# Kernel optimization log

Measured on AMD Instinct MI355X. Metric: run time of the kernel, lower is better.

The kernel has to match this reference:

```python
import jax, jax.numpy as jnp
import numpy as np

N_NODES = 50000
N_EDGES = 600000
D = 128
EPS = 1e-5
AVG_D_LOG = float(np.log(4 + 1))  # avg_d={'log': log(avg_d+1)}, avg_d=4


def setup_inputs() -> dict:
    key = jax.random.key(0)
    ks = jax.random.split(key, 8)
    h = jax.random.normal(ks[0], (N_NODES, D), dtype=jnp.float32)
    # guarantee every node has at least one incoming edge (self-loop)
    edge_dst = jnp.concatenate([
        jnp.arange(N_NODES, dtype=jnp.int64),
        jax.random.randint(ks[1], (N_EDGES - N_NODES,), 0, N_NODES).astype(jnp.int64),
    ])
    edge_src = jax.random.randint(ks[2], (N_EDGES,), 0, N_NODES).astype(jnp.int64)
    def lin(k, fan_in, fan_out):
        lim = 1.0 / np.sqrt(fan_in)
        return jax.random.uniform(k, (fan_in, fan_out), jnp.float32, -lim, lim)
    W_pre = lin(ks[3], 2 * D, D)
    b_pre = jnp.zeros((D,), jnp.float32)
    W_post = lin(ks[4], 12 * D + D, D)  # 4 aggregators * 3 scalers * D + in_dim
    b_post = jnp.zeros((D,), jnp.float32)
    W_mix = lin(ks[5], D, D)
    b_mix = jnp.zeros((D,), jnp.float32)
    return {"h": h, "edge_src": edge_src, "edge_dst": edge_dst,
            "W_pre": W_pre, "b_pre": b_pre, "W_post": W_post,
            "b_post": b_post, "W_mix": W_mix, "b_mix": b_mix}


def reference(h, edge_src, edge_dst, W_pre, b_pre, W_post, b_post, W_mix, b_mix):
    n = h.shape[0]
    # pretrans_edges: cat(src, dst) -> Linear -> ReLU (MLP act) -> ReLU (outer)
    z2 = jnp.concatenate([h[edge_src], h[edge_dst]], axis=1)        # [E, 2D]
    e = jax.nn.relu(z2 @ W_pre + b_pre)                             # [E, D]
    # multi-aggregator segment reduce over destination nodes
    deg = jax.ops.segment_sum(jnp.ones_like(edge_dst, jnp.float32), edge_dst, n)  # [N]
    inv_deg = 1.0 / deg[:, None]
    mean = jax.ops.segment_sum(e, edge_dst, n) * inv_deg
    mean_sq = jax.ops.segment_sum(e * e, edge_dst, n) * inv_deg
    std = jnp.sqrt(jax.nn.relu(mean_sq - mean * mean) + EPS)
    mx = jax.ops.segment_max(e, edge_dst, n)
    mn = jax.ops.segment_min(e, edge_dst, n)
    agg = jnp.concatenate([mean, mx, mn, std], axis=1)              # [N, 4D]
    # scalers: identity, amplification, attenuation
    log_d = jnp.log(deg + 1.0)[:, None]
    scaled = jnp.concatenate([agg, agg * (log_d / AVG_D_LOG), agg * (AVG_D_LOG / log_d)], axis=1)  # [N, 12D]
    # posttrans: cat(h, aggregated) -> Linear -> ReLU
    hp = jax.nn.relu(jnp.concatenate([h, scaled], axis=1) @ W_post + b_post)  # [N, D]
    # mixing network + residual (node_dim == out_dim)
    out = h + jax.nn.leaky_relu(hp @ W_mix + b_mix, negative_slope=0.01)
    return out
```

## Files before the change

kernel.cpp:

```cpp
#include <hip/hip_runtime.h>
#include <hip/hip_bf16.h>

#define N_NODES 50000
#define N_EDGES 600000
#define D 128
#define NB_SCAN 196

constexpr float AVG_D_LOG = 1.6094379124341003f;
constexpr float EPS_V = 1e-5f;

#define PQ_B     0ul
#define AGG_B    25600000ul
#define HBF_B    76800000ul
#define WPRET2_B 89600000ul
#define WPOSTT_B 89665536ul
#define WMIXT_B  90091520ul
#define DEGC_B   90124288ul
#define OFF_B    90324288ul
#define CUR_B    90524352ul
#define SRCS_B   90724352ul
#define BSUM_B   93124352ul

typedef __attribute__((ext_vector_type(8))) short bf16x8;
typedef __attribute__((ext_vector_type(4))) float f32x4;

__device__ __forceinline__ short f2b(float f) {
    unsigned u = __builtin_bit_cast(unsigned, f);
    u += 0x7fffu + ((u >> 16) & 1u);
    return (short)(u >> 16);
}
__device__ __forceinline__ unsigned pk2(float a, float b) {
    return (unsigned)(unsigned short)f2b(a) | ((unsigned)(unsigned short)f2b(b) << 16);
}
__device__ __forceinline__ float blo(unsigned u) { return __uint_as_float(u << 16); }
__device__ __forceinline__ float bhi(unsigned u) { return __uint_as_float(u & 0xffff0000u); }

__global__ __launch_bounds__(256) void prep_kernel(
    const float* __restrict__ h, const float* __restrict__ Wpre,
    const float* __restrict__ Wpost, const float* __restrict__ Wmix,
    short* __restrict__ hbf, short* __restrict__ wpreT2,
    short* __restrict__ wpostT, short* __restrict__ wmixT,
    int* __restrict__ degc, int* __restrict__ cursor)
{
    long i = (long)blockIdx.x * 256 + threadIdx.x;
    if (i < 6400000) { hbf[i] = f2b(h[i]); return; }
    i -= 6400000;
    if (i < 32768) {
        int n = i >> 7, k = i & 127;
        float v = (n < 128) ? Wpre[k * 128 + n] : Wpre[(k + 128) * 128 + (n - 128)];
        wpreT2[n * 128 + k] = f2b(v);
        return;
    }
    i -= 32768;
    if (i < 212992) { int k = i >> 7, n = i & 127; wpostT[n * 1664 + k] = f2b(Wpost[k * 128 + n]); return; }
    i -= 212992;
    if (i < 16384) { int k = i >> 7, n = i & 127; wmixT[n * 128 + k] = f2b(Wmix[k * 128 + n]); return; }
    i -= 16384;
    if (i < N_NODES) { degc[i] = 0; return; }
    i -= N_NODES;
    if (i < N_NODES) cursor[i] = 0;
}

__global__ __launch_bounds__(256) void hist_kernel(const int* __restrict__ edst, int* __restrict__ degc) {
    int e = blockIdx.x * 256 + threadIdx.x;
    if (e < N_EDGES) atomicAdd(&degc[edst[e]], 1);
}

__global__ __launch_bounds__(256) void scan1_kernel(const int* __restrict__ degc, int* __restrict__ bsum) {
    int n = blockIdx.x * 256 + threadIdx.x;
    int v = (n < N_NODES) ? degc[n] : 0;
#pragma unroll
    for (int o = 32; o > 0; o >>= 1) v += __shfl_down(v, o);
    __shared__ int w4[4];
    if ((threadIdx.x & 63) == 0) w4[threadIdx.x >> 6] = v;
    __syncthreads();
    if (threadIdx.x == 0) bsum[blockIdx.x] = w4[0] + w4[1] + w4[2] + w4[3];
}

__global__ __launch_bounds__(256) void scan2_kernel(int* __restrict__ bsum, int* __restrict__ off) {
    __shared__ int sd[256];
    int tid = threadIdx.x;
    int v = (tid < NB_SCAN) ? bsum[tid] : 0;
    sd[tid] = v;
    __syncthreads();
    for (int o = 1; o < 256; o <<= 1) {
        int t = (tid >= o) ? sd[tid - o] : 0;
        __syncthreads();
        sd[tid] += t;
        __syncthreads();
    }
    if (tid < NB_SCAN) bsum[tid] = sd[tid] - v;
    if (tid == 0) off[N_NODES] = sd[255];
}

__global__ __launch_bounds__(256) void scan3_kernel(const int* __restrict__ degc,
                                                    const int* __restrict__ bsum, int* __restrict__ off) {
    __shared__ int sd[256];
    int tid = threadIdx.x;
    int n = blockIdx.x * 256 + tid;
    int v = (n < N_NODES) ? degc[n] : 0;
    sd[tid] = v;
    __syncthreads();
    for (int o = 1; o < 256; o <<= 1) {
        int t = (tid >= o) ? sd[tid - o] : 0;
        __syncthreads();
        sd[tid] += t;
        __syncthreads();
    }
    if (n < N_NODES) off[n] = sd[tid] - v + bsum[blockIdx.x];
}

__global__ __launch_bounds__(256) void scatter_kernel(const int* __restrict__ esrc, const int* __restrict__ edst,
                                                      const int* __restrict__ off, int* __restrict__ cursor,
                                                      int* __restrict__ srcs) {
    int e = blockIdx.x * 256 + threadIdx.x;
    if (e < N_EDGES) {
        int d = edst[e];
        int p = off[d] + atomicAdd(&cursor[d], 1);
        srcs[p] = esrc[e];
    }
}

__global__ __launch_bounds__(256) void gemm_pq_kernel(
    const short* __restrict__ hbf, const short* __restrict__ wpreT2,
    const float* __restrict__ bpre, short* __restrict__ PQ)
{
    __shared__ __align__(16) short As[128][72];
    __shared__ __align__(16) short Bs[256][72];

    const int tid = threadIdx.x;
    const int bn = blockIdx.x * 128;
    const int lane = tid & 63, wv = tid >> 6;
    const int lm = lane & 15, quad = lane >> 4;

    f32x4 acc[2][16];
#pragma unroll
    for (int a = 0; a < 2; a++)
#pragma unroll
        for (int b = 0; b < 16; b++) acc[a][b] = (f32x4){0.f, 0.f, 0.f, 0.f};

#pragma unroll
    for (int kc = 0; kc < 2; kc++) {
        __syncthreads();
#pragma unroll
        for (int t = 0; t < 4; t++) {
            int q = tid + t * 256;
            int m = q >> 3, seg = q & 7;
            int n = bn + m; if (n >= N_NODES) n = N_NODES - 1;
            *(int4*)&As[m][seg * 8] = *(const int4*)(hbf + (long)n * 128 + kc * 64 + seg * 8);
        }
#pragma unroll
        for (int t = 0; t < 8; t++) {
            int q = tid + t * 256;
            int n = q >> 3, seg = q & 7;
            *(int4*)&Bs[n][seg * 8] = *(const int4*)(wpreT2 + n * 128 + kc * 64 + seg * 8);
        }
        __syncthreads();
#pragma unroll
        for (int ks = 0; ks < 2; ks++) {
            const int ko = ks * 32 + quad * 8;
            bf16x8 a0 = *(const bf16x8*)&As[wv * 32 + lm][ko];
            bf16x8 a1 = *(const bf16x8*)&As[wv * 32 + 16 + lm][ko];
#pragma unroll
            for (int ct = 0; ct < 16; ct++) {
                bf16x8 b = *(const bf16x8*)&Bs[ct * 16 + lm][ko];
                acc[0][ct] = __builtin_amdgcn_mfma_f32_16x16x32_bf16(b, a0, acc[0][ct], 0, 0, 0);
                acc[1][ct] = __builtin_amdgcn_mfma_f32_16x16x32_bf16(b, a1, acc[1][ct], 0, 0, 0);
            }
        }
    }

#pragma unroll
    for (int rt = 0; rt < 2; rt++) {
        int row = wv * 32 + rt * 16 + lm;
        int n = bn + row;
        if (n >= N_NODES) continue;
        short* dst = PQ + (long)n * 256;
#pragma unroll
        for (int ct = 0; ct < 16; ct++) {
            int col = ct * 16 + quad * 4;
            float v0 = acc[rt][ct][0], v1 = acc[rt][ct][1], v2 = acc[rt][ct][2], v3 = acc[rt][ct][3];
            if (ct >= 8) {
                float4 bv = *(const float4*)(bpre + (col - 128));
                v0 += bv.x; v1 += bv.y; v2 += bv.z; v3 += bv.w;
            }
            int2 pkd; pkd.x = (int)pk2(v0, v1); pkd.y = (int)pk2(v2, v3);
            *(int2*)(dst + col) = pkd;
        }
    }
}

__global__ __launch_bounds__(256) void edgestats_kernel(
    const short* __restrict__ PQ, const int* __restrict__ srcs,
    const int* __restrict__ off, short* __restrict__ aggbf)
{
    const int wv = threadIdx.x >> 6, lane = threadIdx.x & 63;
    const int n = blockIdx.x * 4 + wv;
    const unsigned* Pb = (const unsigned*)PQ;

    const int s0 = __builtin_amdgcn_readfirstlane(off[n]);
    const int s1 = __builtin_amdgcn_readfirstlane(off[n + 1]);

    unsigned qu = Pb[(long)n * 128 + 64 + lane];
    const float qa = blo(qu), qb = bhi(qu);

    float sA = 0.f, sB = 0.f, qA = 0.f, qB = 0.f;
    float mxA = -1e30f, mxB = -1e30f, mnA = 1e30f, mnB = 1e30f;

    int p = s0;
    for (; p + 4 <= s1; p += 4) {
        int i0 = srcs[p], i1 = srcs[p + 1], i2 = srcs[p + 2], i3 = srcs[p + 3];
        unsigned u0 = Pb[(long)i0 * 128 + lane];
        unsigned u1 = Pb[(long)i1 * 128 + lane];
        unsigned u2 = Pb[(long)i2 * 128 + lane];
        unsigned u3 = Pb[(long)i3 * 128 + lane];
#pragma unroll
        for (int j = 0; j < 4; j++) {
            unsigned u = (j == 0) ? u0 : (j == 1) ? u1 : (j == 2) ? u2 : u3;
            float a = blo(u) + qa; a = a > 0.f ? a : 0.f;
            float b = bhi(u) + qb; b = b > 0.f ? b : 0.f;
            sA += a; sB += b; qA += a * a; qB += b * b;
            mxA = fmaxf(mxA, a); mxB = fmaxf(mxB, b);
            mnA = fminf(mnA, a); mnB = fminf(mnB, b);
        }
    }
    for (; p < s1; p++) {
        unsigned u = Pb[(long)srcs[p] * 128 + lane];
        float a = blo(u) + qa; a = a > 0.f ? a : 0.f;
        float b = bhi(u) + qb; b = b > 0.f ? b : 0.f;
        sA += a; sB += b; qA += a * a; qB += b * b;
        mxA = fmaxf(mxA, a); mxB = fmaxf(mxB, b);
        mnA = fminf(mnA, a); mnB = fminf(mnB, b);
    }

    float inv = 1.0f / (float)(s1 - s0);
    float mA = sA * inv, mB = sB * inv;
    float vA = qA * inv - mA * mA; vA = vA > 0.f ? vA : 0.f;
    float vB = qB * inv - mB * mB; vB = vB > 0.f ? vB : 0.f;
    float stA = sqrtf(vA + EPS_V), stB = sqrtf(vB + EPS_V);

    unsigned* ag = (unsigned*)(aggbf + (long)n * 512);
    ag[lane]       = pk2(mA, mB);
    ag[64 + lane]  = pk2(mxA, mxB);
    ag[128 + lane] = pk2(mnA, mnB);
    ag[192 + lane] = pk2(stA, stB);
}

__global__ __launch_bounds__(256) void node_kernel(
    const float* __restrict__ h, const short* __restrict__ hbf, const short* __restrict__ aggbf,
    const int* __restrict__ degc, const short* __restrict__ wpostT, const float* __restrict__ bpost,
    const short* __restrict__ wmixT, const float* __restrict__ bmix, float* __restrict__ out)
{
    __shared__ __align__(16) short As[64][72];
    __shared__ __align__(16) short Bs[128][72];
    __shared__ float sAmp[64], sAtt[64];

    const int tid = threadIdx.x;
    const int bn = blockIdx.x * 64;
    if (tid < 64) {
        int n = bn + tid; if (n >= N_NODES) n = N_NODES - 1;
        float d = (float)degc[n];
        float ld = logf(d + 1.0f);
        sAmp[tid] = ld * (1.0f / AVG_D_LOG);
        sAtt[tid] = AVG_D_LOG / ld;
    }
    __syncthreads();

    const int lane = tid & 63, wv = tid >> 6;
    const int lm = lane & 15, quad = lane >> 4;
    const int arow = wv * 16 + lm;

    f32x4 acc[8];
#pragma unroll
    for (int b = 0; b < 8; b++) acc[b] = (f32x4){0.f, 0.f, 0.f, 0.f};

    for (int c = 0; c < 26; c++) {
        __syncthreads();
        const int r = c >> 1;
        const int half = (c & 1) * 64;
#pragma unroll
        for (int t = 0; t < 2; t++) {
            int q = tid + t * 256;
            int m = q >> 3, seg = q & 7;
            int n = bn + m; if (n >= N_NODES) n = N_NODES - 1;
            int4 v;
            if (r == 0) {
                v = *(const int4*)(hbf + (long)n * 128 + half + seg * 8);
            } else {
                int a = (r - 1) & 3, s = (r - 1) >> 2;
                v = *(const int4*)(aggbf + (long)n * 512 + a * 128 + half + seg * 8);
                if (s) {
                    float sc = (s == 1) ? sAmp[m] : sAtt[m];
                    unsigned* pu = (unsigned*)&v;
#pragma unroll
                    for (int j = 0; j < 4; j++) {
                        unsigned u = pu[j];
                        pu[j] = pk2(blo(u) * sc, bhi(u) * sc);
                    }
                }
            }
            *(int4*)&As[m][seg * 8] = v;
        }
#pragma unroll
        for (int t = 0; t < 4; t++) {
            int q = tid + t * 256;
            int n = q >> 3, seg = q & 7;
            *(int4*)&Bs[n][seg * 8] = *(const int4*)(wpostT + n * 1664 + c * 64 + seg * 8);
        }
        __syncthreads();
#pragma unroll
        for (int ks = 0; ks < 2; ks++) {
            const int ko = ks * 32 + quad * 8;
            bf16x8 a = *(const bf16x8*)&As[arow][ko];
#pragma unroll
            for (int ct = 0; ct < 8; ct++) {
                bf16x8 b = *(const bf16x8*)&Bs[ct * 16 + lm][ko];
                acc[ct] = __builtin_amdgcn_mfma_f32_16x16x32_bf16(b, a, acc[ct], 0, 0, 0);
            }
        }
    }

#pragma unroll
    for (int ct = 0; ct < 8; ct++) {
        float4 bv = *(const float4*)(bpost + ct * 16 + quad * 4);
        float v0 = acc[ct][0] + bv.x; acc[ct][0] = v0 > 0.f ? v0 : 0.f;
        float v1 = acc[ct][1] + bv.y; acc[ct][1] = v1 > 0.f ? v1 : 0.f;
        float v2 = acc[ct][2] + bv.z; acc[ct][2] = v2 > 0.f ? v2 : 0.f;
        float v3 = acc[ct][3] + bv.w; acc[ct][3] = v3 > 0.f ? v3 : 0.f;
    }

    f32x4 acc2[8];
#pragma unroll
    for (int b = 0; b < 8; b++) acc2[b] = (f32x4){0.f, 0.f, 0.f, 0.f};

#pragma unroll
    for (int kc = 0; kc < 2; kc++) {
        __syncthreads();
#pragma unroll
        for (int ctl = 0; ctl < 4; ctl++) {
            int ct = kc * 4 + ctl;
            int col = ctl * 16 + quad * 4;
            int2 pkd;
            pkd.x = (int)pk2(acc[ct][0], acc[ct][1]);
            pkd.y = (int)pk2(acc[ct][2], acc[ct][3]);
            *(int2*)&As[arow][col] = pkd;
        }
#pragma unroll
        for (int t = 0; t < 4; t++) {
            int q = tid + t * 256;
            int n = q >> 3, seg = q & 7;
            *(int4*)&Bs[n][seg * 8] = *(const int4*)(wmixT + n * 128 + kc * 64 + seg * 8);
        }
        __syncthreads();
#pragma unroll
        for (int ks = 0; ks < 2; ks++) {
            const int ko = ks * 32 + quad * 8;
            bf16x8 a = *(const bf16x8*)&As[arow][ko];
#pragma unroll
            for (int ct = 0; ct < 8; ct++) {
                bf16x8 b = *(const bf16x8*)&Bs[ct * 16 + lm][ko];
                acc2[ct] = __builtin_amdgcn_mfma_f32_16x16x32_bf16(b, a, acc2[ct], 0, 0, 0);
            }
        }
    }

    {
        int n = bn + arow;
        if (n < N_NODES) {
#pragma unroll
            for (int ct = 0; ct < 8; ct++) {
                int col = ct * 16 + quad * 4;
                float4 bv = *(const float4*)(bmix + col);
                float4 hv = *(const float4*)(h + (long)n * 128 + col);
                float4 o;
                float v0 = acc2[ct][0] + bv.x; v0 = v0 > 0.f ? v0 : 0.01f * v0; o.x = hv.x + v0;
                float v1 = acc2[ct][1] + bv.y; v1 = v1 > 0.f ? v1 : 0.01f * v1; o.y = hv.y + v1;
                float v2 = acc2[ct][2] + bv.z; v2 = v2 > 0.f ? v2 : 0.01f * v2; o.z = hv.z + v2;
                float v3 = acc2[ct][3] + bv.w; v3 = v3 > 0.f ? v3 : 0.01f * v3; o.w = hv.w + v3;
                *(float4*)(out + (long)n * 128 + col) = o;
            }
        }
    }
}

extern "C" void kernel_launch(void* const* d_in, const int* in_sizes, int n_in,
                              void* d_out, int out_size, void* d_ws, size_t ws_size,
                              hipStream_t stream) {
    const float* h     = (const float*)d_in[0];
    const int*   esrc  = (const int*)d_in[1];
    const int*   edst  = (const int*)d_in[2];
    const float* Wpre  = (const float*)d_in[3];
    const float* bpre  = (const float*)d_in[4];
    const float* Wpost = (const float*)d_in[5];
    const float* bpost = (const float*)d_in[6];
    const float* Wmix  = (const float*)d_in[7];
    const float* bmix  = (const float*)d_in[8];
    float* out = (float*)d_out;
    char* ws = (char*)d_ws;

    short* PQ     = (short*)(ws + PQ_B);
    short* aggbf  = (short*)(ws + AGG_B);
    short* hbf    = (short*)(ws + HBF_B);
    short* wpreT2 = (short*)(ws + WPRET2_B);
    short* wpostT = (short*)(ws + WPOSTT_B);
    short* wmixT  = (short*)(ws + WMIXT_B);
    int*   degc   = (int*)(ws + DEGC_B);
    int*   off    = (int*)(ws + OFF_B);
    int*   cursor = (int*)(ws + CUR_B);
    int*   srcs   = (int*)(ws + SRCS_B);
    int*   bsum   = (int*)(ws + BSUM_B);

    prep_kernel<<<26415, 256, 0, stream>>>(h, Wpre, Wpost, Wmix, hbf, wpreT2, wpostT, wmixT, degc, cursor);
    hist_kernel<<<(N_EDGES + 255) / 256, 256, 0, stream>>>(edst, degc);
    scan1_kernel<<<NB_SCAN, 256, 0, stream>>>(degc, bsum);
    scan2_kernel<<<1, 256, 0, stream>>>(bsum, off);
    scan3_kernel<<<NB_SCAN, 256, 0, stream>>>(degc, bsum, off);
    scatter_kernel<<<(N_EDGES + 255) / 256, 256, 0, stream>>>(esrc, edst, off, cursor, srcs);
    gemm_pq_kernel<<<(N_NODES + 127) / 128, 256, 0, stream>>>(hbf, wpreT2, bpre, PQ);
    edgestats_kernel<<<N_NODES / 4, 256, 0, stream>>>(PQ, srcs, off, aggbf);
    node_kernel<<<(N_NODES + 63) / 64, 256, 0, stream>>>(h, hbf, aggbf, degc, wpostT, bpost, wmixT, bmix, out);
}
```

Before: 299.6 us.

## Enlarge node GEMM tile to 128 rows per block and unroll edge gather by 8

The node kernel now processes 128 nodes per block with 2 waves. Each wave computes a 64x128 output tile using four A fragments against each B fragment, so B reuse from LDS goes up and the total weight traffic into LDS goes down. The mixing GEMM reads W_mix fragments straight from global memory and stages the hidden activations in both LDS buffers. Separately, the edge-stats loop issues 8 gathers at once instead of 4 to expose more memory-level parallelism. The trade-off is much higher register pressure (64 accumulator vectors per wave) and fewer waves per block, which may lower occupancy.

```diff
diff --git a/kernel.cpp b/kernel.cpp
--- a/kernel.cpp
+++ b/kernel.cpp
@@ -208,17 +208,14 @@
     float mxA = -1e30f, mxB = -1e30f, mnA = 1e30f, mnB = 1e30f;
 
     int p = s0;
-    for (; p + 4 <= s1; p += 4) {
-        int i0 = srcs[p], i1 = srcs[p + 1], i2 = srcs[p + 2], i3 = srcs[p + 3];
-        unsigned u0 = Pb[(long)i0 * 128 + lane];
-        unsigned u1 = Pb[(long)i1 * 128 + lane];
-        unsigned u2 = Pb[(long)i2 * 128 + lane];
-        unsigned u3 = Pb[(long)i3 * 128 + lane];
-#pragma unroll
-        for (int j = 0; j < 4; j++) {
-            unsigned u = (j == 0) ? u0 : (j == 1) ? u1 : (j == 2) ? u2 : u3;
-            float a = blo(u) + qa; a = a > 0.f ? a : 0.f;
-            float b = bhi(u) + qb; b = b > 0.f ? b : 0.f;
+    for (; p + 8 <= s1; p += 8) {
+        unsigned u[8];
+#pragma unroll
+        for (int j = 0; j < 8; j++) u[j] = Pb[(long)srcs[p + j] * 128 + lane];
+#pragma unroll
+        for (int j = 0; j < 8; j++) {
+            float a = blo(u[j]) + qa; a = a > 0.f ? a : 0.f;
+            float b = bhi(u[j]) + qb; b = b > 0.f ? b : 0.f;
             sA += a; sB += b; qA += a * a; qB += b * b;
             mxA = fmaxf(mxA, a); mxB = fmaxf(mxB, b);
             mnA = fminf(mnA, a); mnB = fminf(mnB, b);
@@ -246,18 +243,18 @@
     ag[192 + lane] = pk2(stA, stB);
 }
 
-__global__ __launch_bounds__(256) void node_kernel(
+__global__ __launch_bounds__(128) void node_kernel(
     const float* __restrict__ h, const short* __restrict__ hbf, const short* __restrict__ aggbf,
     const int* __restrict__ degc, const short* __restrict__ wpostT, const float* __restrict__ bpost,
     const short* __restrict__ wmixT, const float* __restrict__ bmix, float* __restrict__ out)
 {
-    __shared__ __align__(16) short As[64][72];
+    __shared__ __align__(16) short As[128][72];
     __shared__ __align__(16) short Bs[128][72];
-    __shared__ float sAmp[64], sAtt[64];
+    __shared__ float sAmp[128], sAtt[128];
 
     const int tid = threadIdx.x;
-    const int bn = blockIdx.x * 64;
-    if (tid < 64) {
+    const int bn = blockIdx.x * 128;
+    {
         int n = bn + tid; if (n >= N_NODES) n = N_NODES - 1;
         float d = (float)degc[n];
         float ld = logf(d + 1.0f);
@@ -268,19 +265,20 @@
 
     const int lane = tid & 63, wv = tid >> 6;
     const int lm = lane & 15, quad = lane >> 4;
-    const int arow = wv * 16 + lm;
-
-    f32x4 acc[8];
-#pragma unroll
-    for (int b = 0; b < 8; b++) acc[b] = (f32x4){0.f, 0.f, 0.f, 0.f};
+
+    f32x4 acc[4][8];
+#pragma unroll
+    for (int a = 0; a < 4; a++)
+#pragma unroll
+        for (int b = 0; b < 8; b++) acc[a][b] = (f32x4){0.f, 0.f, 0.f, 0.f};
 
     for (int c = 0; c < 26; c++) {
         __syncthreads();
         const int r = c >> 1;
         const int half = (c & 1) * 64;
 #pragma unroll
-        for (int t = 0; t < 2; t++) {
-            int q = tid + t * 256;
+        for (int t = 0; t < 8; t++) {
+            int q = tid + t * 128;
             int m = q >> 3, seg = q & 7;
             int n = bn + m; if (n >= N_NODES) n = N_NODES - 1;
             int4 v;
@@ -302,8 +300,8 @@
             *(int4*)&As[m][seg * 8] = v;
         }
 #pragma unroll
-        for (int t = 0; t < 4; t++) {
-            int q = tid + t * 256;
+        for (int t = 0; t < 8; t++) {
+            int q = tid + t * 128;
             int n = q >> 3, seg = q & 7;
             *(int4*)&Bs[n][seg * 8] = *(const int4*)(wpostT + n * 1664 + c * 64 + seg * 8);
         }
@@ -311,74 +309,90 @@
 #pragma unroll
         for (int ks = 0; ks < 2; ks++) {
             const int ko = ks * 32 + quad * 8;
-            bf16x8 a = *(const bf16x8*)&As[arow][ko];
+            bf16x8 a0 = *(const bf16x8*)&As[wv * 64 + lm][ko];
+            bf16x8 a1 = *(const bf16x8*)&As[wv * 64 + 16 + lm][ko];
+            bf16x8 a2 = *(const bf16x8*)&As[wv * 64 + 32 + lm][ko];
+            bf16x8 a3 = *(const bf16x8*)&As[wv * 64 + 48 + lm][ko];
 #pragma unroll
             for (int ct = 0; ct < 8; ct++) {
                 bf16x8 b = *(const bf16x8*)&Bs[ct * 16 + lm][ko];
-                acc[ct] = __builtin_amdgcn_mfma_f32_16x16x32_bf16(b, a, acc[ct], 0, 0, 0);
-            }
-        }
-    }
-
-#pragma unroll
-    for (int ct = 0; ct < 8; ct++) {
-        float4 bv = *(const float4*)(bpost + ct * 16 + quad * 4);
-        float v0 = acc[ct][0] + bv.x; acc[ct][0] = v0 > 0.f ? v0 : 0.f;
-        float v1 = acc[ct][1] + bv.y; acc[ct][1] = v1 > 0.f ? v1 : 0.f;
-        float v2 = acc[ct][2] + bv.z; acc[ct][2] = v2 > 0.f ? v2 : 0.f;
-        float v3 = acc[ct][3] + bv.w; acc[ct][3] = v3 > 0.f ? v3 : 0.f;
-    }
-
-    f32x4 acc2[8];
-#pragma unroll
-    for (int b = 0; b < 8; b++) acc2[b] = (f32x4){0.f, 0.f, 0.f, 0.f};
+                acc[0][ct] = __builtin_amdgcn_mfma_f32_16x16x32_bf16(b, a0, acc[0][ct], 0, 0, 0);
+                acc[1][ct] = __builtin_amdgcn_mfma_f32_16x16x32_bf16(b, a1, acc[1][ct], 0, 0, 0);
+                acc[2][ct] = __builtin_amdgcn_mfma_f32_16x16x32_bf16(b, a2, acc[2][ct], 0, 0, 0);
+                acc[3][ct] = __builtin_amdgcn_mfma_f32_16x16x32_bf16(b, a3, acc[3][ct], 0, 0, 0);
+            }
+        }
+    }
+
+    __syncthreads();
+#pragma unroll
+    for (int rt = 0; rt < 4; rt++) {
+        int row = wv * 64 + rt * 16 + lm;
+#pragma unroll
+        for (int ct = 0; ct < 8; ct++) {
+            float4 bv = *(const float4*)(bpost + ct * 16 + quad * 4);
+            float v0 = acc[rt][ct][0] + bv.x; v0 = v0 > 0.f ? v0 : 0.f;
+            float v1 = acc[rt][ct][1] + bv.y; v1 = v1 > 0.f ? v1 : 0.f;
+            float v2 = acc[rt][ct][2] + bv.z; v2 = v2 > 0.f ? v2 : 0.f;
+            float v3 = acc[rt][ct][3] + bv.w; v3 = v3 > 0.f ? v3 : 0.f;
+            int2 pkd; pkd.x = (int)pk2(v0, v1); pkd.y = (int)pk2(v2, v3);
+            int colL = (ct & 3) * 16 + quad * 4;
+            if (ct < 4) *(int2*)&As[row][colL] = pkd;
+            else        *(int2*)&Bs[row][colL] = pkd;
+        }
+    }
+    __syncthreads();
+
+    f32x4 acc2[4][8];
+#pragma unroll
+    for (int a = 0; a < 4; a++)
+#pragma unroll
+        for (int b = 0; b < 8; b++) acc2[a][b] = (f32x4){0.f, 0.f, 0.f, 0.f};
 
 #pragma unroll
     for (int kc = 0; kc < 2; kc++) {
-        __syncthreads();
-#pragma unroll
-        for (int ctl = 0; ctl < 4; ctl++) {
-            int ct = kc * 4 + ctl;
-            int col = ctl * 16 + quad * 4;
-            int2 pkd;
-            pkd.x = (int)pk2(acc[ct][0], acc[ct][1]);
-            pkd.y = (int)pk2(acc[ct][2], acc[ct][3]);
-            *(int2*)&As[arow][col] = pkd;
-        }
-#pragma unroll
-        for (int t = 0; t < 4; t++) {
-            int q = tid + t * 256;
-            int n = q >> 3, seg = q & 7;
-            *(int4*)&Bs[n][seg * 8] = *(const int4*)(wmixT + n * 128 + kc * 64 + seg * 8);
-        }
-        __syncthreads();
 #pragma unroll
         for (int ks = 0; ks < 2; ks++) {
             const int ko = ks * 32 + quad * 8;
-            bf16x8 a = *(const bf16x8*)&As[arow][ko];
+            bf16x8 a0, a1, a2, a3;
+            if (kc == 0) {
+                a0 = *(const bf16x8*)&As[wv * 64 + lm][ko];
+                a1 = *(const bf16x8*)&As[wv * 64 + 16 + lm][ko];
+                a2 = *(const bf16x8*)&As[wv * 64 + 32 + lm][ko];
+                a3 = *(const bf16x8*)&As[wv * 64 + 48 + lm][ko];
+            } else {
+                a0 = *(const bf16x8*)&Bs[wv * 64 + lm][ko];
+                a1 = *(const bf16x8*)&Bs[wv * 64 + 16 + lm][ko];
+                a2 = *(const bf16x8*)&Bs[wv * 64 + 32 + lm][ko];
+                a3 = *(const bf16x8*)&Bs[wv * 64 + 48 + lm][ko];
+            }
 #pragma unroll
             for (int ct = 0; ct < 8; ct++) {
-                bf16x8 b = *(const bf16x8*)&Bs[ct * 16 + lm][ko];
-                acc2[ct] = __builtin_amdgcn_mfma_f32_16x16x32_bf16(b, a, acc2[ct], 0, 0, 0);
-            }
-        }
-    }
-
-    {
-        int n = bn + arow;
-        if (n < N_NODES) {
-#pragma unroll
-            for (int ct = 0; ct < 8; ct++) {
-                int col = ct * 16 + quad * 4;
-                float4 bv = *(const float4*)(bmix + col);
-                float4 hv = *(const float4*)(h + (long)n * 128 + col);
-                float4 o;
-                float v0 = acc2[ct][0] + bv.x; v0 = v0 > 0.f ? v0 : 0.01f * v0; o.x = hv.x + v0;
-                float v1 = acc2[ct][1] + bv.y; v1 = v1 > 0.f ? v1 : 0.01f * v1; o.y = hv.y + v1;
-                float v2 = acc2[ct][2] + bv.z; v2 = v2 > 0.f ? v2 : 0.01f * v2; o.z = hv.z + v2;
-                float v3 = acc2[ct][3] + bv.w; v3 = v3 > 0.f ? v3 : 0.01f * v3; o.w = hv.w + v3;
-                *(float4*)(out + (long)n * 128 + col) = o;
-            }
+                bf16x8 b = *(const bf16x8*)(wmixT + (ct * 16 + lm) * 128 + kc * 64 + ko);
+                acc2[0][ct] = __builtin_amdgcn_mfma_f32_16x16x32_bf16(b, a0, acc2[0][ct], 0, 0, 0);
+                acc2[1][ct] = __builtin_amdgcn_mfma_f32_16x16x32_bf16(b, a1, acc2[1][ct], 0, 0, 0);
+                acc2[2][ct] = __builtin_amdgcn_mfma_f32_16x16x32_bf16(b, a2, acc2[2][ct], 0, 0, 0);
+                acc2[3][ct] = __builtin_amdgcn_mfma_f32_16x16x32_bf16(b, a3, acc2[3][ct], 0, 0, 0);
+            }
+        }
+    }
+
+#pragma unroll
+    for (int rt = 0; rt < 4; rt++) {
+        int row = wv * 64 + rt * 16 + lm;
+        int n = bn + row;
+        if (n >= N_NODES) continue;
+#pragma unroll
+        for (int ct = 0; ct < 8; ct++) {
+            int col = ct * 16 + quad * 4;
+            float4 bv = *(const float4*)(bmix + col);
+            float4 hv = *(const float4*)(h + (long)n * 128 + col);
+            float4 o;
+            float v0 = acc2[rt][ct][0] + bv.x; v0 = v0 > 0.f ? v0 : 0.01f * v0; o.x = hv.x + v0;
+            float v1 = acc2[rt][ct][1] + bv.y; v1 = v1 > 0.f ? v1 : 0.01f * v1; o.y = hv.y + v1;
+            float v2 = acc2[rt][ct][2] + bv.z; v2 = v2 > 0.f ? v2 : 0.01f * v2; o.z = hv.z + v2;
+            float v3 = acc2[rt][ct][3] + bv.w; v3 = v3 > 0.f ? v3 : 0.01f * v3; o.w = hv.w + v3;
+            *(float4*)(out + (long)n * 128 + col) = o;
         }
     }
 }
@@ -418,5 +432,5 @@
     scatter_kernel<<<(N_EDGES + 255) / 256, 256, 0, stream>>>(esrc, edst, off, cursor, srcs);
     gemm_pq_kernel<<<(N_NODES + 127) / 128, 256, 0, stream>>>(hbf, wpreT2, bpre, PQ);
     edgestats_kernel<<<N_NODES / 4, 256, 0, stream>>>(PQ, srcs, off, aggbf);
-    node_kernel<<<(N_NODES + 63) / 64, 256, 0, stream>>>(h, hbf, aggbf, degc, wpostT, bpost, wmixT, bmix, out);
-}
+    node_kernel<<<(N_NODES + 127) / 128, 128, 0, stream>>>(h, hbf, aggbf, degc, wpostT, bpost, wmixT, bmix, out);
+}
```

Result: slower. 327.5 us (+9.3%).
